# Kernel optimization log

Hardware: AMD Instinct MI355X
Metric: run time of the kernel (lower is better)

## Reference

```python
import jax, jax.numpy as jnp
import numpy as np

NUM_KERNELS = 6
ALPHA = 0.5
DIL = 9
FEAT = 4
DELTA_V = 0.5
DELTA_D = 1.5
EMB_W = 0.25
MAX_LABELS = 16


def setup_inputs() -> dict:
    key = jax.random.key(0)
    k1, k2, k3, k4, k5 = jax.random.split(key, 5)
    B, H, W = 8, 640, 640
    pred = jax.random.normal(k1, (B, NUM_KERNELS + FEAT, H, W), dtype=jnp.float32)
    gt_text = (jax.random.uniform(k2, (B, 1, H, W)) < 0.3).astype(jnp.float32)
    gt_kernels = (jax.random.uniform(k3, (B, NUM_KERNELS - 1, H, W)) < 0.2).astype(jnp.float32)
    training_mask = (jax.random.uniform(k4, (B, 1, H, W)) > 0.05).astype(jnp.float32)
    gt_instance = jax.random.randint(k5, (B, H, W), 0, MAX_LABELS, dtype=jnp.int32)
    return {"pred": pred, "gt_text": gt_text, "gt_kernels": gt_kernels,
            "training_mask": training_mask, "gt_instance": gt_instance}


def _dice(inp, tgt, msk, eps=1e-6):
    # inp/tgt/msk: [N, HW]; returns mean over N of (1 - 2*I/U)
    inp = inp * msk
    tgt = tgt * msk
    inter = (inp * tgt).sum(1)
    union = (inp ** 2).sum(1) + (tgt ** 2).sum(1) + eps
    return (1.0 - 2.0 * inter / union).mean()


def _ohem(pred, gt, tm, ratio=3):
    # Vectorized OHEM: keep all positives + top-(3*n_pos) hardest negatives per sample.
    B = gt.shape[0]
    p = pred.reshape(B, -1)
    g = gt.reshape(B, -1)
    m = tm.reshape(B, -1)
    pos = (g > 0.5) & (m > 0.5)
    neg = (g <= 0.5) & (m > 0.5)
    n_pos = pos.sum(1)
    n_neg = jnp.minimum(ratio * n_pos, neg.sum(1))
    score = jnp.where(neg, p, -jnp.inf)
    # rank[i,j] = position of element j in descending order of score[i]
    rank = jnp.argsort(jnp.argsort(-score, axis=1), axis=1)
    mask = pos | (neg & (rank < n_neg[:, None]))
    return mask.astype(pred.dtype).reshape(gt.shape)


def _emb_sample(emb, gt, tm):
    # emb: [D,H,W], gt: [H,W] int, tm: [H,W]
    D = emb.shape[0]
    e = emb.reshape(D, -1).T                       # [HW, D]
    g = gt.reshape(-1)
    valid = tm.reshape(-1) > 0
    ids = jnp.where(valid, g, MAX_LABELS)          # invalid pixels -> dump segment
    ones = valid.astype(e.dtype)
    counts = jax.ops.segment_sum(ones, ids, num_segments=MAX_LABELS + 1)[:MAX_LABELS]
    sums = jax.ops.segment_sum(e * ones[:, None], ids, num_segments=MAX_LABELS + 1)[:MAX_LABELS]
    present = counts > 0
    n = present.sum()
    nf = n.astype(e.dtype)
    means = sums / jnp.maximum(counts, 1.0)[:, None]   # [L, D]
    # variance term: per-pixel distance to own cluster mean
    own = means[g]                                     # [HW, D]
    d = jnp.sqrt(((e - own) ** 2).sum(1) + 1e-12)
    cv = jnp.maximum(d - DELTA_V, 0.0) ** 2
    per = jax.ops.segment_sum(cv * ones, ids, num_segments=MAX_LABELS + 1)[:MAX_LABELS]
    per = per / jnp.maximum(counts, 1.0)
    lv = jnp.where(present, per, 0.0).sum() / jnp.maximum(nf, 1.0)
    # distance term: pairwise over present cluster means (unordered pairs i<j)
    diff = means[:, None, :] - means[None, :, :]
    pd = jnp.sqrt((diff ** 2).sum(-1) + 1e-12)
    iu = jnp.arange(MAX_LABELS)
    pm = present[:, None] & present[None, :] & (iu[:, None] < iu[None, :])
    ld = jnp.where(pm, jnp.maximum(2.0 * DELTA_D - pd, 0.0) ** 2, 0.0).sum()
    ld = ld / jnp.maximum(nf * (nf - 1.0), 1.0)
    # regularization: mean norm of present cluster means
    lr = jnp.where(present, jnp.sqrt((means ** 2).sum(1) + 1e-12), 0.0).sum() / jnp.maximum(nf, 1.0)
    act = (n > 1).astype(e.dtype)   # skip samples with <=1 instance (matches `continue`)
    return act * lv, act * ld, act * lr


def reference(pred, gt_text, gt_kernels, training_mask, gt_instance):
    B = pred.shape[0]
    gt_t = gt_text[:, 0]
    tm = training_mask[:, 0]
    # text branch: sigmoid -> 9x9 max-pool dilation -> OHEM dice
    prob = jax.nn.sigmoid(pred[:, 0])
    pad = DIL // 2
    dil = jax.lax.reduce_window(prob, -jnp.inf, jax.lax.max,
                                (1, DIL, DIL), (1, 1, 1),
                                [(0, 0), (pad, pad), (pad, pad)])
    ohem = jax.lax.stop_gradient(_ohem(dil, gt_t, tm, ratio=3))
    loss_text = _dice(dil.reshape(B, -1), gt_t.reshape(B, -1), ohem.reshape(B, -1))
    # kernel branch: mean over (B, K) equals sum_k dice_k / K
    K = NUM_KERNELS - 1
    pk = jax.nn.sigmoid(pred[:, 1:NUM_KERNELS]).reshape(B * K, -1)
    gk = gt_kernels.reshape(B * K, -1)
    mk = jnp.broadcast_to(tm[:, None], (B, K) + tm.shape[1:]).reshape(B * K, -1)
    loss_kernels = _dice(pk, gk, mk)
    # embedding clustering loss
    pred_emb = pred[:, NUM_KERNELS:]
    lv, ld, lr = jax.vmap(_emb_sample)(pred_emb, gt_instance, tm)
    loss_emb = EMB_W * (lv.sum() + ld.sum() + 0.001 * (lr.sum() / B))
    loss = loss_kernels + ALPHA * loss_text + loss_emb
    return loss, loss_text, loss_kernels, loss_emb
```

## Files before the change

### kernel.cpp

```cpp
#include <hip/hip_runtime.h>
#include <math.h>

#define BB 8
#define HH 640
#define WW 640
#define HWN (HH*WW)
#define CC 10
#define KCH 5
#define DD 4
#define LL 16
#define NBINS 256

#define WS_OHEM      0
#define WS_HCNT      64
#define WS_HS2       (WS_HCNT + BB*NBINS)
#define WS_KERN      (WS_HS2 + BB*NBINS)
#define WS_ECNT      (WS_KERN + 120)
#define WS_ESUM      (WS_ECNT + BB*LL)
#define WS_ECV       (WS_ESUM + BB*LL*DD)
#define WS_ZERO_END  (WS_ECV + BB)
#define WS_MEANS     WS_ZERO_END
#define WS_INVC      (WS_MEANS + BB*LL*DD)
#define WS_MISC      (WS_INVC + BB*LL)

__device__ __forceinline__ float sigm(float x) { return 1.f / (1.f + expf(-x)); }

__device__ __forceinline__ float wave_red(float v) {
    #pragma unroll
    for (int o = 32; o > 0; o >>= 1) v += __shfl_down(v, o);
    return v;
}

__device__ __forceinline__ float4 ld4g(const float* __restrict__ p, int row, int cb) {
    float4 v;
    if (row < 0 || row >= HH) { v.x = v.y = v.z = v.w = -INFINITY; return v; }
    const float* rp = p + (size_t)row * WW;
    if (cb >= 0 && cb <= WW - 4) return *(const float4*)(rp + cb);
    v.x = ((unsigned)(cb + 0) < (unsigned)WW) ? rp[cb + 0] : -INFINITY;
    v.y = ((unsigned)(cb + 1) < (unsigned)WW) ? rp[cb + 1] : -INFINITY;
    v.z = ((unsigned)(cb + 2) < (unsigned)WW) ? rp[cb + 2] : -INFINITY;
    v.w = ((unsigned)(cb + 3) < (unsigned)WW) ? rp[cb + 3] : -INFINITY;
    return v;
}

__global__ __launch_bounds__(256) void k_dil_stats(
    const float* __restrict__ pred, const float* __restrict__ gt_t,
    const float* __restrict__ tm, float* __restrict__ ws)
{
    __shared__ float hmax[72][65];
    __shared__ float hcnt[2][NBINS];
    __shared__ float hs2[2][NBINS];
    __shared__ float red[8];
    const int b  = blockIdx.z;
    const int x0 = blockIdx.x * 64;
    const int y0 = blockIdx.y * 64;
    const int tid = threadIdx.x;
    const float* p0 = pred + (size_t)b * CC * HWN;

    for (int i = tid; i < 2 * NBINS; i += 256) {
        ((float*)hcnt)[i] = 0.f; ((float*)hs2)[i] = 0.f;
    }
    if (tid < 8) red[tid] = 0.f;

    for (int i = tid; i < 72 * 16; i += 256) {
        int r = i >> 4, g = i & 15;
        int gr = y0 + r - 4;
        int cb = x0 + 4 * g - 4;
        float4 A = ld4g(p0, gr, cb);
        float4 Bv = ld4g(p0, gr, cb + 4);
        float4 Cv = ld4g(p0, gr, cb + 8);
        float s3 = A.w;
        float s2 = fmaxf(A.z, s3);
        float s1 = fmaxf(A.y, s2);
        float s0 = fmaxf(A.x, s1);
        float mid = fmaxf(fmaxf(Bv.x, Bv.y), fmaxf(Bv.z, Bv.w));
        float q0 = Cv.x;
        float q1 = fmaxf(q0, Cv.y);
        float q2 = fmaxf(q1, Cv.z);
        float q3 = fmaxf(q2, Cv.w);
        int c = 4 * g;
        hmax[r][c + 0] = fmaxf(fmaxf(s0, mid), q0);
        hmax[r][c + 1] = fmaxf(fmaxf(s1, mid), q1);
        hmax[r][c + 2] = fmaxf(fmaxf(s2, mid), q2);
        hmax[r][c + 3] = fmaxf(fmaxf(s3, mid), q3);
    }
    __syncthreads();

    const int c  = tid & 63;
    const int rb = tid >> 6;
    const int hc = tid >> 7;
    float c_pos = 0.f, s_pos = 0.f, s_pos2 = 0.f, c_neg = 0.f, s_neg2 = 0.f;
    #pragma unroll
    for (int k = 0; k < 16; k++) {
        int r = rb * 16 + k;
        float m = hmax[r][c];
        #pragma unroll
        for (int j = 1; j < 9; j++) m = fmaxf(m, hmax[r + j][c]);
        float dil = sigm(m);
        size_t gidx = (size_t)b * HWN + (size_t)(y0 + r) * WW + (x0 + c);
        float g = gt_t[gidx], mv = tm[gidx];
        if (mv > 0.5f) {
            if (g > 0.5f) { c_pos += 1.f; s_pos += dil; s_pos2 += dil * dil; }
            else {
                c_neg += 1.f; s_neg2 += dil * dil;
                int bin = (int)((m + 8.f) * 16.f);
                bin = min(max(bin, 0), NBINS - 1);
                atomicAdd(&hcnt[hc][bin], 1.f);
                atomicAdd(&hs2[hc][bin], dil * dil);
            }
        }
    }
    c_pos = wave_red(c_pos); s_pos = wave_red(s_pos); s_pos2 = wave_red(s_pos2);
    c_neg = wave_red(c_neg); s_neg2 = wave_red(s_neg2);
    if ((tid & 63) == 0) {
        atomicAdd(&red[0], c_pos);  atomicAdd(&red[1], s_pos);
        atomicAdd(&red[2], s_pos2); atomicAdd(&red[3], c_neg);
        atomicAdd(&red[4], s_neg2);
    }
    __syncthreads();
    float* oh = ws + WS_OHEM + b * 8;
    if (tid < 5) atomicAdd(&oh[tid], red[tid]);
    float* gh_c = ws + WS_HCNT + b * NBINS;
    float* gh_s = ws + WS_HS2  + b * NBINS;
    for (int i = tid; i < NBINS; i += 256) {
        float sc = hcnt[0][i] + hcnt[1][i];
        if (sc != 0.f) {
            atomicAdd(&gh_c[i], sc);
            atomicAdd(&gh_s[i], hs2[0][i] + hs2[1][i]);
        }
    }
}

__global__ __launch_bounds__(256) void k_kern_dice(
    const float* __restrict__ pred, const float* __restrict__ gtk,
    const float* __restrict__ tm, float* __restrict__ ws)
{
    const int row = blockIdx.y;
    const int b = row / KCH, k = row - b * KCH;
    const float4* p = (const float4*)(pred + ((size_t)b * CC + 1 + k) * HWN);
    const float4* g = (const float4*)(gtk + (size_t)row * HWN);
    const float4* m = (const float4*)(tm + (size_t)b * HWN);
    const int nv = HWN / 4;
    float i1 = 0.f, i2 = 0.f, i3 = 0.f;
    for (int j = blockIdx.x * 256 + threadIdx.x; j < nv; j += gridDim.x * 256) {
        float4 pv = p[j], gv = g[j], mv = m[j];
        float s0 = sigm(pv.x), s1 = sigm(pv.y), s2 = sigm(pv.z), s3 = sigm(pv.w);
        i1 += s0*gv.x*mv.x + s1*gv.y*mv.y + s2*gv.z*mv.z + s3*gv.w*mv.w;
        i2 += s0*s0*mv.x + s1*s1*mv.y + s2*s2*mv.z + s3*s3*mv.w;
        i3 += gv.x*mv.x + gv.y*mv.y + gv.z*mv.z + gv.w*mv.w;
    }
    i1 = wave_red(i1); i2 = wave_red(i2); i3 = wave_red(i3);
    __shared__ float sred[12];
    int wv = threadIdx.x >> 6;
    if ((threadIdx.x & 63) == 0) { sred[wv*3] = i1; sred[wv*3+1] = i2; sred[wv*3+2] = i3; }
    __syncthreads();
    if (threadIdx.x == 0) {
        float a = 0.f, bb = 0.f, c = 0.f;
        for (int w = 0; w < 4; w++) { a += sred[w*3]; bb += sred[w*3+1]; c += sred[w*3+2]; }
        float* kk = ws + WS_KERN + row * 3;
        atomicAdd(&kk[0], a); atomicAdd(&kk[1], bb); atomicAdd(&kk[2], c);
    }
}

__global__ __launch_bounds__(256) void k_emb1(
    const float* __restrict__ pred, const int* __restrict__ inst,
    const float* __restrict__ tm, float* __restrict__ ws)
{
    const int b = blockIdx.y;
    const int tid = threadIdx.x;
    const float* e0 = pred + ((size_t)b * CC + 6) * HWN;
    const float4* v0p = (const float4*)e0;
    const float4* v1p = (const float4*)(e0 + HWN);
    const float4* v2p = (const float4*)(e0 + 2 * HWN);
    const float4* v3p = (const float4*)(e0 + 3 * HWN);
    const float4* tmv = (const float4*)(tm + (size_t)b * HWN);
    const int4*   iv  = (const int4*)(inst + (size_t)b * HWN);

    float cnt[LL], s0[LL], s1[LL], s2[LL], s3[LL];
    #pragma unroll
    for (int l = 0; l < LL; l++) { cnt[l]=0.f; s0[l]=0.f; s1[l]=0.f; s2[l]=0.f; s3[l]=0.f; }

    const int nv = HWN / 4;
    for (int j = blockIdx.x * 256 + tid; j < nv; j += gridDim.x * 256) {
        float4 a0 = v0p[j], a1 = v1p[j], a2 = v2p[j], a3 = v3p[j];
        float4 t = tmv[j];
        int4 li = iv[j];
        int lab0 = (t.x > 0.f) ? li.x : LL;
        int lab1 = (t.y > 0.f) ? li.y : LL;
        int lab2 = (t.z > 0.f) ? li.z : LL;
        int lab3 = (t.w > 0.f) ? li.w : LL;
        #pragma unroll
        for (int l = 0; l < LL; l++) {
            float m0 = (lab0 == l) ? 1.f : 0.f;
            float m1 = (lab1 == l) ? 1.f : 0.f;
            float m2 = (lab2 == l) ? 1.f : 0.f;
            float m3 = (lab3 == l) ? 1.f : 0.f;
            cnt[l] += (m0 + m1) + (m2 + m3);
            s0[l] += m0*a0.x + m1*a0.y + m2*a0.z + m3*a0.w;
            s1[l] += m0*a1.x + m1*a1.y + m2*a1.z + m3*a1.w;
            s2[l] += m0*a2.x + m1*a2.y + m2*a2.z + m3*a2.w;
            s3[l] += m0*a3.x + m1*a3.y + m2*a3.z + m3*a3.w;
        }
    }

    __shared__ float sred[4][80];
    const int wv = tid >> 6, ln = tid & 63;
    #pragma unroll
    for (int l = 0; l < LL; l++) {
        float r0 = wave_red(cnt[l]);
        float r1 = wave_red(s0[l]);
        float r2 = wave_red(s1[l]);
        float r3 = wave_red(s2[l]);
        float r4 = wave_red(s3[l]);
        if (ln == 0) {
            sred[wv][l*5+0] = r0; sred[wv][l*5+1] = r1; sred[wv][l*5+2] = r2;
            sred[wv][l*5+3] = r3; sred[wv][l*5+4] = r4;
        }
    }
    __syncthreads();
    if (tid < 80) {
        float s = sred[0][tid] + sred[1][tid] + sred[2][tid] + sred[3][tid];
        int l = tid / 5, c = tid - l * 5;
        if (c == 0) atomicAdd(&ws[WS_ECNT + b * LL + l], s);
        else        atomicAdd(&ws[WS_ESUM + b * LL * DD + l * DD + (c - 1)], s);
    }
}

__global__ __launch_bounds__(128) void k_emb_means(float* __restrict__ ws)
{
    const int b = blockIdx.x;
    __shared__ float mn[LL][DD];
    __shared__ float pres[LL];
    __shared__ float redp[128];
    __shared__ float redr[LL];
    const int tid = threadIdx.x;
    if (tid < LL) {
        float c = ws[WS_ECNT + b * LL + tid];
        float inv = 1.f / fmaxf(c, 1.f);
        ws[WS_INVC + b * LL + tid] = inv;
        #pragma unroll
        for (int d = 0; d < DD; d++) {
            float mv = ws[WS_ESUM + b * LL * DD + tid * DD + d] * inv;
            mn[tid][d] = mv;
            ws[WS_MEANS + b * LL * DD + tid * DD + d] = mv;
        }
        pres[tid] = (c > 0.f) ? 1.f : 0.f;
    }
    __syncthreads();
    float ldv = 0.f;
    if (tid < 120) {
        int idx = tid, ii = 0;
        while (idx >= (LL - 1 - ii)) { idx -= (LL - 1 - ii); ii++; }
        int jj = ii + 1 + idx;
        float s = 1e-12f;
        #pragma unroll
        for (int d = 0; d < DD; d++) { float df = mn[ii][d] - mn[jj][d]; s += df * df; }
        float pd = sqrtf(s);
        float t = fmaxf(3.0f - pd, 0.f);
        ldv = (pres[ii] > 0.f && pres[jj] > 0.f) ? t * t : 0.f;
    }
    redp[tid] = ldv;
    float lrv = 0.f;
    if (tid < LL && pres[tid] > 0.f) {
        float s = 1e-12f;
        #pragma unroll
        for (int d = 0; d < DD; d++) s += mn[tid][d] * mn[tid][d];
        lrv = sqrtf(s);
    }
    if (tid < LL) redr[tid] = lrv;
    __syncthreads();
    if (tid == 0) {
        float nf = 0.f;
        for (int i = 0; i < LL; i++) nf += pres[i];
        float ld = 0.f;
        for (int i = 0; i < 120; i++) ld += redp[i];
        float lr = 0.f;
        for (int i = 0; i < LL; i++) lr += redr[i];
        float act = (nf > 1.f) ? 1.f : 0.f;
        ld = act * ld / fmaxf(nf * (nf - 1.f), 1.f);
        lr = act * lr / fmaxf(nf, 1.f);
        ws[WS_MISC + b * 4 + 0] = nf;
        ws[WS_MISC + b * 4 + 1] = ld;
        ws[WS_MISC + b * 4 + 2] = lr;
        ws[WS_MISC + b * 4 + 3] = act;
    }
}

__global__ __launch_bounds__(256) void k_emb2(
    const float* __restrict__ pred, const int* __restrict__ inst,
    const float* __restrict__ tm, float* __restrict__ ws)
{
    const int b = blockIdx.y;
    const int tid = threadIdx.x;
    __shared__ float mn[LL * DD];
    __shared__ float invc[LL];
    if (tid < LL * DD) mn[tid] = ws[WS_MEANS + b * LL * DD + tid];
    if (tid < LL) invc[tid] = ws[WS_INVC + b * LL + tid];
    __syncthreads();

    const float* e0 = pred + ((size_t)b * CC + 6) * HWN;
    const float4* v0p = (const float4*)e0;
    const float4* v1p = (const float4*)(e0 + HWN);
    const float4* v2p = (const float4*)(e0 + 2 * HWN);
    const float4* v3p = (const float4*)(e0 + 3 * HWN);
    const float4* tmv = (const float4*)(tm + (size_t)b * HWN);
    const int4*   iv  = (const int4*)(inst + (size_t)b * HWN);

    float acc = 0.f;
    const int nv = HWN / 4;
    for (int j = blockIdx.x * 256 + tid; j < nv; j += gridDim.x * 256) {
        float4 a0 = v0p[j], a1 = v1p[j], a2 = v2p[j], a3 = v3p[j];
        float4 t = tmv[j];
        int4 li = iv[j];
        float ex[4] = {a0.x, a0.y, a0.z, a0.w};
        float ey[4] = {a1.x, a1.y, a1.z, a1.w};
        float ez[4] = {a2.x, a2.y, a2.z, a2.w};
        float ew[4] = {a3.x, a3.y, a3.z, a3.w};
        int   lb[4] = {li.x, li.y, li.z, li.w};
        float tv[4] = {t.x, t.y, t.z, t.w};
        #pragma unroll
        for (int q = 0; q < 4; q++) {
            int l = lb[q];
            float d0 = ex[q] - mn[l * DD + 0];
            float d1 = ey[q] - mn[l * DD + 1];
            float d2 = ez[q] - mn[l * DD + 2];
            float d3 = ew[q] - mn[l * DD + 3];
            float dd = sqrtf(d0*d0 + d1*d1 + d2*d2 + d3*d3 + 1e-12f);
            float tt = fmaxf(dd - 0.5f, 0.f);
            float w = (tv[q] > 0.f) ? invc[l] : 0.f;
            acc += w * tt * tt;
        }
    }

    acc = wave_red(acc);
    __shared__ float sred[4];
    const int wv = tid >> 6;
    if ((tid & 63) == 0) sred[wv] = acc;
    __syncthreads();
    if (tid == 0)
        atomicAdd(&ws[WS_ECV + b], sred[0] + sred[1] + sred[2] + sred[3]);
}

__global__ __launch_bounds__(64) void k_final(const float* __restrict__ ws, float* __restrict__ out)
{
    __shared__ float s_text[BB];
    __shared__ float s_kern[40];
    __shared__ float s_lv[BB], s_ld[BB], s_lr[BB];
    const int tid = threadIdx.x;
    if (tid < BB) {
        const float* o = ws + WS_OHEM + tid * 8;
        float npos = o[0], spos = o[1], spos2 = o[2], nnegt = o[3], sneg2t = o[4];
        float nneg = fminf(3.f * npos, nnegt);
        float ssel;
        if (nneg >= nnegt) ssel = sneg2t;
        else {
            const float* hcn = ws + WS_HCNT + tid * NBINS;
            const float* hs = ws + WS_HS2  + tid * NBINS;
            float acc = 0.f; ssel = 0.f;
            for (int i = NBINS - 1; i >= 0; i--) {
                float c = hcn[i];
                if (c <= 0.f) continue;
                if (acc + c <= nneg) { ssel += hs[i]; acc += c; }
                else { float r = nneg - acc; ssel += r * (hs[i] / c); break; }
            }
        }
        float uni = spos2 + ssel + npos + 1e-6f;
        s_text[tid] = 1.f - 2.f * spos / uni;

        float nf  = ws[WS_MISC + tid * 4 + 0];
        float act = ws[WS_MISC + tid * 4 + 3];
        s_lv[tid] = act * ws[WS_ECV + tid] / fmaxf(nf, 1.f);
        s_ld[tid] = ws[WS_MISC + tid * 4 + 1];
        s_lr[tid] = ws[WS_MISC + tid * 4 + 2];
    }
    if (tid < 40) {
        const float* kk = ws + WS_KERN + tid * 3;
        s_kern[tid] = 1.f - 2.f * kk[0] / (kk[1] + kk[2] + 1e-6f);
    }
    __syncthreads();
    if (tid == 0) {
        float lt = 0.f; for (int i = 0; i < BB; i++) lt += s_text[i]; lt /= (float)BB;
        float lk = 0.f; for (int i = 0; i < 40; i++) lk += s_kern[i]; lk /= 40.f;
        float lvs = 0.f, lds_ = 0.f, lrs = 0.f;
        for (int i = 0; i < BB; i++) { lvs += s_lv[i]; lds_ += s_ld[i]; lrs += s_lr[i]; }
        float lemb = 0.25f * (lvs + lds_ + 0.001f * (lrs / (float)BB));
        out[0] = lk + 0.5f * lt + lemb;
        out[1] = lt;
        out[2] = lk;
        out[3] = lemb;
    }
}

extern "C" void kernel_launch(void* const* d_in, const int* in_sizes, int n_in,
                              void* d_out, int out_size, void* d_ws, size_t ws_size,
                              hipStream_t stream)
{
    (void)in_sizes; (void)n_in; (void)out_size; (void)ws_size;
    const float* pred = (const float*)d_in[0];
    const float* gt_t = (const float*)d_in[1];
    const float* gtk  = (const float*)d_in[2];
    const float* tm   = (const float*)d_in[3];
    const int*   inst = (const int*)d_in[4];
    float* out = (float*)d_out;
    float* ws  = (float*)d_ws;

    hipMemsetAsync(d_ws, 0, WS_ZERO_END * sizeof(float), stream);

    dim3 g1(WW / 64, HH / 64, BB), b1(256, 1, 1);
    k_dil_stats<<<g1, b1, 0, stream>>>(pred, gt_t, tm, ws);
    k_kern_dice<<<dim3(48, 40), 256, 0, stream>>>(pred, gtk, tm, ws);
    k_emb1<<<dim3(96, BB), 256, 0, stream>>>(pred, inst, tm, ws);
    k_emb_means<<<BB, 128, 0, stream>>>(ws);
    k_emb2<<<dim3(128, BB), 256, 0, stream>>>(pred, inst, tm, ws);
    k_final<<<1, 64, 0, stream>>>(ws, out);
}
```

Before: 354.8 us.

## Fuse dilation stats, kernel dice and embedding pass-1 into one launch

Merges three independent streaming kernels into a single kernel whose blocks branch on blockIdx to run the dilation/OHEM histogram, the kernel dice, or the first embedding pass. It also changes the grid splits: 640 dice blocks instead of 1920 and 512 embedding blocks instead of 768. The aim is to cut launch gaps and tail effects by letting the different workloads overlap on the GPU. In exchange, every block now reserves the larger shared-memory footprint and the register usage of the heaviest branch, which can lower occupancy for the light dice blocks.

Result: slower. 402.1 us (+13.3%).

```diff
diff --git a/kernel.cpp b/kernel.cpp
--- a/kernel.cpp
+++ b/kernel.cpp
@@ -10,6 +10,10 @@
 #define DD 4
 #define LL 16
 #define NBINS 256
+
+#define NDIL  800
+#define NDICE 640
+#define NEMB1 512
 
 #define WS_OHEM      0
 #define WS_HCNT      64
@@ -43,186 +47,184 @@
     return v;
 }
 
-__global__ __launch_bounds__(256) void k_dil_stats(
+__global__ __launch_bounds__(256) void k_fused(
     const float* __restrict__ pred, const float* __restrict__ gt_t,
-    const float* __restrict__ tm, float* __restrict__ ws)
+    const float* __restrict__ gtk,  const float* __restrict__ tm,
+    const int*   __restrict__ inst, float* __restrict__ ws)
 {
-    __shared__ float hmax[72][65];
-    __shared__ float hcnt[2][NBINS];
-    __shared__ float hs2[2][NBINS];
-    __shared__ float red[8];
-    const int b  = blockIdx.z;
-    const int x0 = blockIdx.x * 64;
-    const int y0 = blockIdx.y * 64;
+    __shared__ float smem[72 * 65 + 4 * NBINS + 8];
     const int tid = threadIdx.x;
-    const float* p0 = pred + (size_t)b * CC * HWN;
-
-    for (int i = tid; i < 2 * NBINS; i += 256) {
-        ((float*)hcnt)[i] = 0.f; ((float*)hs2)[i] = 0.f;
-    }
-    if (tid < 8) red[tid] = 0.f;
-
-    for (int i = tid; i < 72 * 16; i += 256) {
-        int r = i >> 4, g = i & 15;
-        int gr = y0 + r - 4;
-        int cb = x0 + 4 * g - 4;
-        float4 A = ld4g(p0, gr, cb);
-        float4 Bv = ld4g(p0, gr, cb + 4);
-        float4 Cv = ld4g(p0, gr, cb + 8);
-        float s3 = A.w;
-        float s2 = fmaxf(A.z, s3);
-        float s1 = fmaxf(A.y, s2);
-        float s0 = fmaxf(A.x, s1);
-        float mid = fmaxf(fmaxf(Bv.x, Bv.y), fmaxf(Bv.z, Bv.w));
-        float q0 = Cv.x;
-        float q1 = fmaxf(q0, Cv.y);
-        float q2 = fmaxf(q1, Cv.z);
-        float q3 = fmaxf(q2, Cv.w);
-        int c = 4 * g;
-        hmax[r][c + 0] = fmaxf(fmaxf(s0, mid), q0);
-        hmax[r][c + 1] = fmaxf(fmaxf(s1, mid), q1);
-        hmax[r][c + 2] = fmaxf(fmaxf(s2, mid), q2);
-        hmax[r][c + 3] = fmaxf(fmaxf(s3, mid), q3);
-    }
-    __syncthreads();
-
-    const int c  = tid & 63;
-    const int rb = tid >> 6;
-    const int hc = tid >> 7;
-    float c_pos = 0.f, s_pos = 0.f, s_pos2 = 0.f, c_neg = 0.f, s_neg2 = 0.f;
-    #pragma unroll
-    for (int k = 0; k < 16; k++) {
-        int r = rb * 16 + k;
-        float m = hmax[r][c];
-        #pragma unroll
-        for (int j = 1; j < 9; j++) m = fmaxf(m, hmax[r + j][c]);
-        float dil = sigm(m);
-        size_t gidx = (size_t)b * HWN + (size_t)(y0 + r) * WW + (x0 + c);
-        float g = gt_t[gidx], mv = tm[gidx];
-        if (mv > 0.5f) {
-            if (g > 0.5f) { c_pos += 1.f; s_pos += dil; s_pos2 += dil * dil; }
-            else {
-                c_neg += 1.f; s_neg2 += dil * dil;
-                int bin = (int)((m + 8.f) * 16.f);
-                bin = min(max(bin, 0), NBINS - 1);
-                atomicAdd(&hcnt[hc][bin], 1.f);
-                atomicAdd(&hs2[hc][bin], dil * dil);
+    const int blk = blockIdx.x;
+
+    if (blk < NDIL) {
+        float* hmax = smem;
+        float* hcnt = smem + 72 * 65;
+        float* hs2  = hcnt + 2 * NBINS;
+        float* red  = hs2 + 2 * NBINS;
+        const int b  = blk / 100;
+        const int rem = blk - b * 100;
+        const int y0 = (rem / 10) * 64;
+        const int x0 = (rem - (rem / 10) * 10) * 64;
+        const float* p0 = pred + (size_t)b * CC * HWN;
+
+        for (int i = tid; i < 4 * NBINS; i += 256) { hcnt[i] = 0.f; }
+        if (tid < 8) red[tid] = 0.f;
+
+        for (int i = tid; i < 72 * 16; i += 256) {
+            int r = i >> 4, g = i & 15;
+            int gr = y0 + r - 4;
+            int cb = x0 + 4 * g - 4;
+            float4 A  = ld4g(p0, gr, cb);
+            float4 Bv = ld4g(p0, gr, cb + 4);
+            float4 Cv = ld4g(p0, gr, cb + 8);
+            float s3 = A.w;
+            float s2 = fmaxf(A.z, s3);
+            float s1 = fmaxf(A.y, s2);
+            float s0 = fmaxf(A.x, s1);
+            float mid = fmaxf(fmaxf(Bv.x, Bv.y), fmaxf(Bv.z, Bv.w));
+            float q0 = Cv.x;
+            float q1 = fmaxf(q0, Cv.y);
+            float q2 = fmaxf(q1, Cv.z);
+            float q3 = fmaxf(q2, Cv.w);
+            int c = 4 * g;
+            hmax[r * 65 + c + 0] = fmaxf(fmaxf(s0, mid), q0);
+            hmax[r * 65 + c + 1] = fmaxf(fmaxf(s1, mid), q1);
+            hmax[r * 65 + c + 2] = fmaxf(fmaxf(s2, mid), q2);
+            hmax[r * 65 + c + 3] = fmaxf(fmaxf(s3, mid), q3);
+        }
+        __syncthreads();
+
+        const int c  = tid & 63;
+        const int rb = tid >> 6;
+        const int hc = (tid >> 7) * NBINS;
+        float c_pos = 0.f, s_pos = 0.f, s_pos2 = 0.f, c_neg = 0.f, s_neg2 = 0.f;
+        #pragma unroll
+        for (int k = 0; k < 16; k++) {
+            int r = rb * 16 + k;
+            float m = hmax[r * 65 + c];
+            #pragma unroll
+            for (int j = 1; j < 9; j++) m = fmaxf(m, hmax[(r + j) * 65 + c]);
+            float dil = sigm(m);
+            size_t gidx = (size_t)b * HWN + (size_t)(y0 + r) * WW + (x0 + c);
+            float g = gt_t[gidx], mv = tm[gidx];
+            if (mv > 0.5f) {
+                if (g > 0.5f) { c_pos += 1.f; s_pos += dil; s_pos2 += dil * dil; }
+                else {
+                    c_neg += 1.f; s_neg2 += dil * dil;
+                    int bin = (int)((m + 8.f) * 16.f);
+                    bin = min(max(bin, 0), NBINS - 1);
+                    atomicAdd(&hcnt[hc + bin], 1.f);
+                    atomicAdd(&hs2[hc + bin], dil * dil);
+                }
             }
         }
-    }
-    c_pos = wave_red(c_pos); s_pos = wave_red(s_pos); s_pos2 = wave_red(s_pos2);
-    c_neg = wave_red(c_neg); s_neg2 = wave_red(s_neg2);
-    if ((tid & 63) == 0) {
-        atomicAdd(&red[0], c_pos);  atomicAdd(&red[1], s_pos);
-        atomicAdd(&red[2], s_pos2); atomicAdd(&red[3], c_neg);
-        atomicAdd(&red[4], s_neg2);
-    }
-    __syncthreads();
-    float* oh = ws + WS_OHEM + b * 8;
-    if (tid < 5) atomicAdd(&oh[tid], red[tid]);
-    float* gh_c = ws + WS_HCNT + b * NBINS;
-    float* gh_s = ws + WS_HS2  + b * NBINS;
-    for (int i = tid; i < NBINS; i += 256) {
-        float sc = hcnt[0][i] + hcnt[1][i];
-        if (sc != 0.f) {
-            atomicAdd(&gh_c[i], sc);
-            atomicAdd(&gh_s[i], hs2[0][i] + hs2[1][i]);
-        }
-    }
-}
-
-__global__ __launch_bounds__(256) void k_kern_dice(
-    const float* __restrict__ pred, const float* __restrict__ gtk,
-    const float* __restrict__ tm, float* __restrict__ ws)
-{
-    const int row = blockIdx.y;
-    const int b = row / KCH, k = row - b * KCH;
-    const float4* p = (const float4*)(pred + ((size_t)b * CC + 1 + k) * HWN);
-    const float4* g = (const float4*)(gtk + (size_t)row * HWN);
-    const float4* m = (const float4*)(tm + (size_t)b * HWN);
-    const int nv = HWN / 4;
-    float i1 = 0.f, i2 = 0.f, i3 = 0.f;
-    for (int j = blockIdx.x * 256 + threadIdx.x; j < nv; j += gridDim.x * 256) {
-        float4 pv = p[j], gv = g[j], mv = m[j];
-        float s0 = sigm(pv.x), s1 = sigm(pv.y), s2 = sigm(pv.z), s3 = sigm(pv.w);
-        i1 += s0*gv.x*mv.x + s1*gv.y*mv.y + s2*gv.z*mv.z + s3*gv.w*mv.w;
-        i2 += s0*s0*mv.x + s1*s1*mv.y + s2*s2*mv.z + s3*s3*mv.w;
-        i3 += gv.x*mv.x + gv.y*mv.y + gv.z*mv.z + gv.w*mv.w;
-    }
-    i1 = wave_red(i1); i2 = wave_red(i2); i3 = wave_red(i3);
-    __shared__ float sred[12];
-    int wv = threadIdx.x >> 6;
-    if ((threadIdx.x & 63) == 0) { sred[wv*3] = i1; sred[wv*3+1] = i2; sred[wv*3+2] = i3; }
-    __syncthreads();
-    if (threadIdx.x == 0) {
-        float a = 0.f, bb = 0.f, c = 0.f;
-        for (int w = 0; w < 4; w++) { a += sred[w*3]; bb += sred[w*3+1]; c += sred[w*3+2]; }
-        float* kk = ws + WS_KERN + row * 3;
-        atomicAdd(&kk[0], a); atomicAdd(&kk[1], bb); atomicAdd(&kk[2], c);
-    }
-}
-
-__global__ __launch_bounds__(256) void k_emb1(
-    const float* __restrict__ pred, const int* __restrict__ inst,
-    const float* __restrict__ tm, float* __restrict__ ws)
-{
-    const int b = blockIdx.y;
-    const int tid = threadIdx.x;
-    const float* e0 = pred + ((size_t)b * CC + 6) * HWN;
-    const float4* v0p = (const float4*)e0;
-    const float4* v1p = (const float4*)(e0 + HWN);
-    const float4* v2p = (const float4*)(e0 + 2 * HWN);
-    const float4* v3p = (const float4*)(e0 + 3 * HWN);
-    const float4* tmv = (const float4*)(tm + (size_t)b * HWN);
-    const int4*   iv  = (const int4*)(inst + (size_t)b * HWN);
-
-    float cnt[LL], s0[LL], s1[LL], s2[LL], s3[LL];
-    #pragma unroll
-    for (int l = 0; l < LL; l++) { cnt[l]=0.f; s0[l]=0.f; s1[l]=0.f; s2[l]=0.f; s3[l]=0.f; }
-
-    const int nv = HWN / 4;
-    for (int j = blockIdx.x * 256 + tid; j < nv; j += gridDim.x * 256) {
-        float4 a0 = v0p[j], a1 = v1p[j], a2 = v2p[j], a3 = v3p[j];
-        float4 t = tmv[j];
-        int4 li = iv[j];
-        int lab0 = (t.x > 0.f) ? li.x : LL;
-        int lab1 = (t.y > 0.f) ? li.y : LL;
-        int lab2 = (t.z > 0.f) ? li.z : LL;
-        int lab3 = (t.w > 0.f) ? li.w : LL;
+        c_pos = wave_red(c_pos); s_pos = wave_red(s_pos); s_pos2 = wave_red(s_pos2);
+        c_neg = wave_red(c_neg); s_neg2 = wave_red(s_neg2);
+        if ((tid & 63) == 0) {
+            atomicAdd(&red[0], c_pos);  atomicAdd(&red[1], s_pos);
+            atomicAdd(&red[2], s_pos2); atomicAdd(&red[3], c_neg);
+            atomicAdd(&red[4], s_neg2);
+        }
+        __syncthreads();
+        float* oh = ws + WS_OHEM + b * 8;
+        if (tid < 5) atomicAdd(&oh[tid], red[tid]);
+        float* gh_c = ws + WS_HCNT + b * NBINS;
+        float* gh_s = ws + WS_HS2  + b * NBINS;
+        for (int i = tid; i < NBINS; i += 256) {
+            float sc = hcnt[i] + hcnt[NBINS + i];
+            if (sc != 0.f) {
+                atomicAdd(&gh_c[i], sc);
+                atomicAdd(&gh_s[i], hs2[i] + hs2[NBINS + i]);
+            }
+        }
+    } else if (blk < NDIL + NDICE) {
+        const int d = blk - NDIL;
+        const int row = d >> 4;
+        const int xb  = d & 15;
+        const int b = row / KCH, k = row - b * KCH;
+        const float4* p = (const float4*)(pred + ((size_t)b * CC + 1 + k) * HWN);
+        const float4* g = (const float4*)(gtk + (size_t)row * HWN);
+        const float4* m = (const float4*)(tm + (size_t)b * HWN);
+        const int nv = HWN / 4;
+        float i1 = 0.f, i2 = 0.f, i3 = 0.f;
+        for (int j = xb * 256 + tid; j < nv; j += 16 * 256) {
+            float4 pv = p[j], gv = g[j], mv = m[j];
+            float s0 = sigm(pv.x), s1 = sigm(pv.y), s2 = sigm(pv.z), s3 = sigm(pv.w);
+            i1 += s0*gv.x*mv.x + s1*gv.y*mv.y + s2*gv.z*mv.z + s3*gv.w*mv.w;
+            i2 += s0*s0*mv.x + s1*s1*mv.y + s2*s2*mv.z + s3*s3*mv.w;
+            i3 += gv.x*mv.x + gv.y*mv.y + gv.z*mv.z + gv.w*mv.w;
+        }
+        i1 = wave_red(i1); i2 = wave_red(i2); i3 = wave_red(i3);
+        float* sred = smem;
+        int wv = tid >> 6;
+        if ((tid & 63) == 0) { sred[wv*3] = i1; sred[wv*3+1] = i2; sred[wv*3+2] = i3; }
+        __syncthreads();
+        if (tid == 0) {
+            float a = 0.f, bb = 0.f, c = 0.f;
+            for (int w = 0; w < 4; w++) { a += sred[w*3]; bb += sred[w*3+1]; c += sred[w*3+2]; }
+            float* kk = ws + WS_KERN + row * 3;
+            atomicAdd(&kk[0], a); atomicAdd(&kk[1], bb); atomicAdd(&kk[2], c);
+        }
+    } else {
+        const int e = blk - NDIL - NDICE;
+        const int b  = e >> 6;
+        const int xb = e & 63;
+        const float* e0 = pred + ((size_t)b * CC + 6) * HWN;
+        const float4* v0p = (const float4*)e0;
+        const float4* v1p = (const float4*)(e0 + HWN);
+        const float4* v2p = (const float4*)(e0 + 2 * HWN);
+        const float4* v3p = (const float4*)(e0 + 3 * HWN);
+        const float4* tmv = (const float4*)(tm + (size_t)b * HWN);
+        const int4*   iv  = (const int4*)(inst + (size_t)b * HWN);
+
+        float cnt[LL], s0[LL], s1[LL], s2[LL], s3[LL];
+        #pragma unroll
+        for (int l = 0; l < LL; l++) { cnt[l]=0.f; s0[l]=0.f; s1[l]=0.f; s2[l]=0.f; s3[l]=0.f; }
+
+        const int nv = HWN / 4;
+        for (int j = xb * 256 + tid; j < nv; j += 64 * 256) {
+            float4 a0 = v0p[j], a1 = v1p[j], a2 = v2p[j], a3 = v3p[j];
+            float4 t = tmv[j];
+            int4 li = iv[j];
+            int lab0 = (t.x > 0.f) ? li.x : LL;
+            int lab1 = (t.y > 0.f) ? li.y : LL;
+            int lab2 = (t.z > 0.f) ? li.z : LL;
+            int lab3 = (t.w > 0.f) ? li.w : LL;
+            #pragma unroll
+            for (int l = 0; l < LL; l++) {
+                float m0 = (lab0 == l) ? 1.f : 0.f;
+                float m1 = (lab1 == l) ? 1.f : 0.f;
+                float m2 = (lab2 == l) ? 1.f : 0.f;
+                float m3 = (lab3 == l) ? 1.f : 0.f;
+                cnt[l] += (m0 + m1) + (m2 + m3);
+                s0[l] += m0*a0.x + m1*a0.y + m2*a0.z + m3*a0.w;
+                s1[l] += m0*a1.x + m1*a1.y + m2*a1.z + m3*a1.w;
+                s2[l] += m0*a2.x + m1*a2.y + m2*a2.z + m3*a2.w;
+                s3[l] += m0*a3.x + m1*a3.y + m2*a3.z + m3*a3.w;
+            }
+        }
+
+        float* sred = smem;
+        const int wv = tid >> 6, ln = tid & 63;
         #pragma unroll
         for (int l = 0; l < LL; l++) {
-            float m0 = (lab0 == l) ? 1.f : 0.f;
-            float m1 = (lab1 == l) ? 1.f : 0.f;
-            float m2 = (lab2 == l) ? 1.f : 0.f;
-            float m3 = (lab3 == l) ? 1.f : 0.f;
-            cnt[l] += (m0 + m1) + (m2 + m3);
-            s0[l] += m0*a0.x + m1*a0.y + m2*a0.z + m3*a0.w;
-            s1[l] += m0*a1.x + m1*a1.y + m2*a1.z + m3*a1.w;
-            s2[l] += m0*a2.x + m1*a2.y + m2*a2.z + m3*a2.w;
-            s3[l] += m0*a3.x + m1*a3.y + m2*a3.z + m3*a3.w;
-        }
-    }
-
-    __shared__ float sred[4][80];
-    const int wv = tid >> 6, ln = tid & 63;
-    #pragma unroll
-    for (int l = 0; l < LL; l++) {
-        float r0 = wave_red(cnt[l]);
-        float r1 = wave_red(s0[l]);
-        float r2 = wave_red(s1[l]);
-        float r3 = wave_red(s2[l]);
-        float r4 = wave_red(s3[l]);
-        if (ln == 0) {
-            sred[wv][l*5+0] = r0; sred[wv][l*5+1] = r1; sred[wv][l*5+2] = r2;
-            sred[wv][l*5+3] = r3; sred[wv][l*5+4] = r4;
-        }
-    }
-    __syncthreads();
-    if (tid < 80) {
-        float s = sred[0][tid] + sred[1][tid] + sred[2][tid] + sred[3][tid];
-        int l = tid / 5, c = tid - l * 5;
-        if (c == 0) atomicAdd(&ws[WS_ECNT + b * LL + l], s);
-        else        atomicAdd(&ws[WS_ESUM + b * LL * DD + l * DD + (c - 1)], s);
+            float r0 = wave_red(cnt[l]);
+            float r1 = wave_red(s0[l]);
+            float r2 = wave_red(s1[l]);
+            float r3 = wave_red(s2[l]);
+            float r4 = wave_red(s3[l]);
+            if (ln == 0) {
+                sred[wv*80 + l*5+0] = r0; sred[wv*80 + l*5+1] = r1; sred[wv*80 + l*5+2] = r2;
+                sred[wv*80 + l*5+3] = r3; sred[wv*80 + l*5+4] = r4;
+            }
+        }
+        __syncthreads();
+        if (tid < 80) {
+            float s = sred[tid] + sred[80 + tid] + sred[160 + tid] + sred[240 + tid];
+            int l = tid / 5, c = tid - l * 5;
+            if (c == 0) atomicAdd(&ws[WS_ECNT + b * LL + l], s);
+            else        atomicAdd(&ws[WS_ESUM + b * LL * DD + l * DD + (c - 1)], s);
+        }
     }
 }
 
@@ -406,10 +408,7 @@
 
     hipMemsetAsync(d_ws, 0, WS_ZERO_END * sizeof(float), stream);
 
-    dim3 g1(WW / 64, HH / 64, BB), b1(256, 1, 1);
-    k_dil_stats<<<g1, b1, 0, stream>>>(pred, gt_t, tm, ws);
-    k_kern_dice<<<dim3(48, 40), 256, 0, stream>>>(pred, gtk, tm, ws);
-    k_emb1<<<dim3(96, BB), 256, 0, stream>>>(pred, inst, tm, ws);
+    k_fused<<<NDIL + NDICE + NEMB1, 256, 0, stream>>>(pred, gt_t, gtk, tm, inst, ws);
     k_emb_means<<<BB, 128, 0, stream>>>(ws);
     k_emb2<<<dim3(128, BB), 256, 0, stream>>>(pred, inst, tm, ws);
     k_final<<<1, 64, 0, stream>>>(ws, out);
```

## Compute embedding segment sums with bf16 MFMA one-hot matmul

Applied to the files above, without the earlier changes.

Rewrites the per-label count/sum accumulation in k_emb1 as a matrix product: pixel tiles are staged in shared memory as bf16 embeddings plus masked labels, and each wave builds one-hot label rows to feed mfma_f32_16x16x32_bf16, with count and channel sums as B columns. This replaces the 16-label unrolled compare/FMA loop and its large register footprint. The trade-off is bf16 rounding of embedding values in the sums, which changes precision, plus shared-memory staging and barriers per tile; the grid also shrinks from 96 to 64 blocks per batch.

New measurement: 338.1 us. 1.05x faster.

```diff
diff --git a/kernel.cpp b/kernel.cpp
--- a/kernel.cpp
+++ b/kernel.cpp
@@ -10,6 +10,7 @@
 #define DD 4
 #define LL 16
 #define NBINS 256
+#define ETILE 1024
 
 #define WS_OHEM      0
 #define WS_HCNT      64
@@ -23,12 +24,19 @@
 #define WS_INVC      (WS_MEANS + BB*LL*DD)
 #define WS_MISC      (WS_INVC + BB*LL)
 
+typedef short bf16x8 __attribute__((ext_vector_type(8)));
+typedef float f32x4  __attribute__((ext_vector_type(4)));
+
 __device__ __forceinline__ float sigm(float x) { return 1.f / (1.f + expf(-x)); }
 
 __device__ __forceinline__ float wave_red(float v) {
     #pragma unroll
     for (int o = 32; o > 0; o >>= 1) v += __shfl_down(v, o);
     return v;
+}
+
+__device__ __forceinline__ unsigned short f2bf(float x) {
+    return (unsigned short)((__float_as_uint(x) + 0x8000u) >> 16);
 }
 
 __device__ __forceinline__ float4 ld4g(const float* __restrict__ p, int row, int cb) {
@@ -66,7 +74,7 @@
         int r = i >> 4, g = i & 15;
         int gr = y0 + r - 4;
         int cb = x0 + 4 * g - 4;
-        float4 A = ld4g(p0, gr, cb);
+        float4 A  = ld4g(p0, gr, cb);
         float4 Bv = ld4g(p0, gr, cb + 4);
         float4 Cv = ld4g(p0, gr, cb + 8);
         float s3 = A.w;
@@ -167,59 +175,79 @@
     const float* __restrict__ tm, float* __restrict__ ws)
 {
     const int b = blockIdx.y;
-    const int tid = threadIdx.x;
-    const float* e0 = pred + ((size_t)b * CC + 6) * HWN;
-    const float4* v0p = (const float4*)e0;
-    const float4* v1p = (const float4*)(e0 + HWN);
-    const float4* v2p = (const float4*)(e0 + 2 * HWN);
-    const float4* v3p = (const float4*)(e0 + 3 * HWN);
-    const float4* tmv = (const float4*)(tm + (size_t)b * HWN);
-    const int4*   iv  = (const int4*)(inst + (size_t)b * HWN);
-
-    float cnt[LL], s0[LL], s1[LL], s2[LL], s3[LL];
-    #pragma unroll
-    for (int l = 0; l < LL; l++) { cnt[l]=0.f; s0[l]=0.f; s1[l]=0.f; s2[l]=0.f; s3[l]=0.f; }
-
-    const int nv = HWN / 4;
-    for (int j = blockIdx.x * 256 + tid; j < nv; j += gridDim.x * 256) {
-        float4 a0 = v0p[j], a1 = v1p[j], a2 = v2p[j], a3 = v3p[j];
-        float4 t = tmv[j];
-        int4 li = iv[j];
-        int lab0 = (t.x > 0.f) ? li.x : LL;
-        int lab1 = (t.y > 0.f) ? li.y : LL;
-        int lab2 = (t.z > 0.f) ? li.z : LL;
-        int lab3 = (t.w > 0.f) ? li.w : LL;
-        #pragma unroll
-        for (int l = 0; l < LL; l++) {
-            float m0 = (lab0 == l) ? 1.f : 0.f;
-            float m1 = (lab1 == l) ? 1.f : 0.f;
-            float m2 = (lab2 == l) ? 1.f : 0.f;
-            float m3 = (lab3 == l) ? 1.f : 0.f;
-            cnt[l] += (m0 + m1) + (m2 + m3);
-            s0[l] += m0*a0.x + m1*a0.y + m2*a0.z + m3*a0.w;
-            s1[l] += m0*a1.x + m1*a1.y + m2*a1.z + m3*a1.w;
-            s2[l] += m0*a2.x + m1*a2.y + m2*a2.z + m3*a2.w;
-            s3[l] += m0*a3.x + m1*a3.y + m2*a3.z + m3*a3.w;
-        }
-    }
-
-    __shared__ float sred[4][80];
-    const int wv = tid >> 6, ln = tid & 63;
-    #pragma unroll
-    for (int l = 0; l < LL; l++) {
-        float r0 = wave_red(cnt[l]);
-        float r1 = wave_red(s0[l]);
-        float r2 = wave_red(s1[l]);
-        float r3 = wave_red(s2[l]);
-        float r4 = wave_red(s3[l]);
-        if (ln == 0) {
-            sred[wv][l*5+0] = r0; sred[wv][l*5+1] = r1; sred[wv][l*5+2] = r2;
-            sred[wv][l*5+3] = r3; sred[wv][l*5+4] = r4;
-        }
+    __shared__ unsigned short chs[4][ETILE + 16];
+    __shared__ unsigned int   labv[ETILE];
+    __shared__ float          merge[4 * 80];
+    const int tid  = threadIdx.x;
+    const int wave = tid >> 6, lane = tid & 63;
+    const int q = lane >> 4, n = lane & 15;
+    const float* e0  = pred + ((size_t)b * CC + 6) * HWN;
+    const float* tmb = tm + (size_t)b * HWN;
+    const int*   ib  = inst + (size_t)b * HWN;
+
+    const bool isch = (n >= 1 && n <= 4);
+    const int  cn   = isch ? (n - 1) : 0;
+
+    f32x4 acc = {0.f, 0.f, 0.f, 0.f};
+
+    for (int t0 = blockIdx.x * ETILE; t0 < HWN; t0 += gridDim.x * ETILE) {
+        {
+            int p = t0 + tid * 4;
+            float4 T = *(const float4*)(tmb + p);
+            int4   L = *(const int4*)(ib + p);
+            #pragma unroll
+            for (int c = 0; c < 4; c++) {
+                float4 V = *(const float4*)(e0 + (size_t)c * HWN + p);
+                unsigned short* dst = &chs[c][tid * 4];
+                dst[0] = f2bf(V.x); dst[1] = f2bf(V.y);
+                dst[2] = f2bf(V.z); dst[3] = f2bf(V.w);
+            }
+            uint4 lv;
+            lv.x = (T.x > 0.f) ? (unsigned)L.x : 255u;
+            lv.y = (T.y > 0.f) ? (unsigned)L.y : 255u;
+            lv.z = (T.z > 0.f) ? (unsigned)L.z : 255u;
+            lv.w = (T.w > 0.f) ? (unsigned)L.w : 255u;
+            *(uint4*)&labv[tid * 4] = lv;
+        }
+        __syncthreads();
+
+        for (int c2 = wave; c2 < ETILE / 32; c2 += 4) {
+            const int base = c2 * 32 + q * 8;
+            uint4 La = *(const uint4*)&labv[base];
+            uint4 Lb = *(const uint4*)&labv[base + 4];
+            union { unsigned short u[8]; bf16x8 v; } A_;
+            const unsigned un = (unsigned)n;
+            A_.u[0] = (La.x == un) ? 0x3F80 : 0;
+            A_.u[1] = (La.y == un) ? 0x3F80 : 0;
+            A_.u[2] = (La.z == un) ? 0x3F80 : 0;
+            A_.u[3] = (La.w == un) ? 0x3F80 : 0;
+            A_.u[4] = (Lb.x == un) ? 0x3F80 : 0;
+            A_.u[5] = (Lb.y == un) ? 0x3F80 : 0;
+            A_.u[6] = (Lb.z == un) ? 0x3F80 : 0;
+            A_.u[7] = (Lb.w == un) ? 0x3F80 : 0;
+            bf16x8 Bf;
+            if (isch) {
+                Bf = *(const bf16x8*)&chs[cn][base];
+            } else if (n == 0) {
+                #pragma unroll
+                for (int j = 0; j < 8; j++) Bf[j] = (short)0x3F80;
+            } else {
+                #pragma unroll
+                for (int j = 0; j < 8; j++) Bf[j] = 0;
+            }
+            acc = __builtin_amdgcn_mfma_f32_16x16x32_bf16(A_.v, Bf, acc, 0, 0, 0);
+        }
+        __syncthreads();
+    }
+
+    if (n <= 4) {
+        #pragma unroll
+        for (int r = 0; r < 4; r++)
+            merge[wave * 80 + (q * 4 + r) * 5 + n] = acc[r];
     }
     __syncthreads();
     if (tid < 80) {
-        float s = sred[0][tid] + sred[1][tid] + sred[2][tid] + sred[3][tid];
+        float s = merge[tid] + merge[80 + tid] + merge[160 + tid] + merge[240 + tid];
         int l = tid / 5, c = tid - l * 5;
         if (c == 0) atomicAdd(&ws[WS_ECNT + b * LL + l], s);
         else        atomicAdd(&ws[WS_ESUM + b * LL * DD + l * DD + (c - 1)], s);
@@ -319,15 +347,15 @@
         int   lb[4] = {li.x, li.y, li.z, li.w};
         float tv[4] = {t.x, t.y, t.z, t.w};
         #pragma unroll
-        for (int q = 0; q < 4; q++) {
-            int l = lb[q];
-            float d0 = ex[q] - mn[l * DD + 0];
-            float d1 = ey[q] - mn[l * DD + 1];
-            float d2 = ez[q] - mn[l * DD + 2];
-            float d3 = ew[q] - mn[l * DD + 3];
+        for (int qq = 0; qq < 4; qq++) {
+            int l = lb[qq];
+            float d0 = ex[qq] - mn[l * DD + 0];
+            float d1 = ey[qq] - mn[l * DD + 1];
+            float d2 = ez[qq] - mn[l * DD + 2];
+            float d3 = ew[qq] - mn[l * DD + 3];
             float dd = sqrtf(d0*d0 + d1*d1 + d2*d2 + d3*d3 + 1e-12f);
             float tt = fmaxf(dd - 0.5f, 0.f);
-            float w = (tv[q] > 0.f) ? invc[l] : 0.f;
+            float w = (tv[qq] > 0.f) ? invc[l] : 0.f;
             acc += w * tt * tt;
         }
     }
@@ -409,7 +437,7 @@
     dim3 g1(WW / 64, HH / 64, BB), b1(256, 1, 1);
     k_dil_stats<<<g1, b1, 0, stream>>>(pred, gt_t, tm, ws);
     k_kern_dice<<<dim3(48, 40), 256, 0, stream>>>(pred, gtk, tm, ws);
-    k_emb1<<<dim3(96, BB), 256, 0, stream>>>(pred, inst, tm, ws);
+    k_emb1<<<dim3(64, BB), 256, 0, stream>>>(pred, inst, tm, ws);
     k_emb_means<<<BB, 128, 0, stream>>>(ws);
     k_emb2<<<dim3(128, BB), 256, 0, stream>>>(pred, inst, tm, ws);
     k_final<<<1, 64, 0, stream>>>(ws, out);
```
